# Kernel optimization log

Measured on AMD Instinct MI355X. Metric: run time of the kernel, lower is better.

Reference implementation:

```python
import jax, jax.numpy as jnp
import numpy as np

B, S, H = 1, 4096, 2048
NH, NKV, HD = 8, 4, 256
I = 8192
EPS = 1e-6
THETA = 10000.0
WINDOW = 4096  # hardcoded sliding window for even layer_idx
LAYER_IDX = 0


def rms_norm(x, w):
    v = jnp.mean(jnp.square(x), axis=-1, keepdims=True)
    return x * jax.lax.rsqrt(v + EPS) * w


def rotate_half(x):
    h = x.shape[-1] // 2
    return jnp.concatenate([-x[..., h:], x[..., :h]], axis=-1)


def apply_rope(q, k, positions):
    # q: [B,S,NH,HD], k: [B,S,NKV,HD], positions: [B,S]
    inv_freq = 1.0 / (THETA ** (jnp.arange(0, HD, 2, dtype=jnp.float32) / HD))
    freqs = positions.astype(jnp.float32)[..., None] * inv_freq  # [B,S,HD/2]
    emb = jnp.concatenate([freqs, freqs], axis=-1)               # [B,S,HD]
    cos = jnp.cos(emb)[:, :, None, :]
    sin = jnp.sin(emb)[:, :, None, :]
    q = q * cos + rotate_half(q) * sin
    k = k * cos + rotate_half(k) * sin
    return q, k


def forward(hidden_states, q_w, k_w, v_w, o_w, gate_w, up_w, down_w, ln1_w, ln2_w,
            attention_mask, position_ids):
    # ---- input RMSNorm + attention ----
    residual = hidden_states
    x = rms_norm(hidden_states, ln1_w)

    q = (x @ q_w).reshape(B, S, NH, HD)
    k = (x @ k_w).reshape(B, S, NKV, HD)
    v = (x @ v_w).reshape(B, S, NKV, HD)
    q, k = apply_rope(q, k, position_ids)

    # GQA: repeat kv heads to match query heads
    groups = NH // NKV
    k = jnp.repeat(k, groups, axis=2)  # [B,S,NH,HD]
    v = jnp.repeat(v, groups, axis=2)

    # masks: padding mask AND causal AND (even layer) local window of WINDOW
    row = jnp.arange(S)[:, None]
    col = jnp.arange(S)[None, :]
    causal = col <= row                                   # [S,S]
    combined = causal[None, None] & (attention_mask[:, None, None, :] > 0)
    if LAYER_IDX % 2 == 0:
        keep = ~(col <= row - WINDOW)                     # mask out keys older than WINDOW
        combined = combined & keep[None, None]
    neg = jnp.finfo(jnp.float32).min
    bias = jnp.where(combined, 0.0, neg).astype(jnp.float32)  # [B,1,S,S]

    scale = HD ** -0.5
    scores = jnp.einsum('bqhd,bkhd->bhqk', q, k) * scale + bias
    probs = jax.nn.softmax(scores, axis=-1)
    attn = jnp.einsum('bhqk,bkhd->bqhd', probs, v).reshape(B, S, NH * HD)
    attn_out = attn @ o_w

    hidden_states = residual + attn_out

    # ---- post-attention RMSNorm + gated-GeLU MLP ----
    residual = hidden_states
    x = rms_norm(hidden_states, ln2_w)
    mlp = (jax.nn.gelu(x @ gate_w, approximate=True) * (x @ up_w)) @ down_w
    return residual + mlp


def setup_inputs() -> dict:
    key = jax.random.key(0)
    ks = jax.random.split(key, 9)
    std = 0.02
    n = lambda k, shp: jax.random.normal(k, shp, dtype=jnp.float32) * std
    return {
        'hidden_states': jax.random.normal(ks[0], (B, S, H), dtype=jnp.float32),
        'q_w': n(ks[1], (H, NH * HD)),
        'k_w': n(ks[2], (H, NKV * HD)),
        'v_w': n(ks[3], (H, NKV * HD)),
        'o_w': n(ks[4], (NH * HD, H)),
        'gate_w': n(ks[5], (H, I)),
        'up_w': n(ks[6], (H, I)),
        'down_w': n(ks[7], (I, H)),
        'ln1_w': jnp.ones((H,), jnp.float32),
        'ln2_w': jnp.ones((H,), jnp.float32),
        'attention_mask': jnp.ones((B, S), jnp.int32),
        'position_ids': jnp.broadcast_to(jnp.arange(S, dtype=jnp.int32)[None, :], (B, S)),
    }


def reference(hidden_states, q_w, k_w, v_w, o_w, gate_w, up_w, down_w, ln1_w, ln2_w,
              attention_mask, position_ids):
    return forward(hidden_states, q_w, k_w, v_w, o_w, gate_w, up_w, down_w,
                   ln1_w, ln2_w, attention_mask, position_ids)
```

## Files before the change

### kernel.cpp

```cpp
#include <hip/hip_runtime.h>
#include <hip/hip_bf16.h>
#include <math.h>

#define S_LEN 4096
#define HID   2048
#define NHEADS 8
#define NKVH   4
#define HDIM   256
#define FFN    8192
#define WIN    4096

typedef __bf16 bf16_t;
typedef __bf16 bf16x4 __attribute__((ext_vector_type(4)));
typedef __bf16 bf16x8 __attribute__((ext_vector_type(8)));
typedef float  floatx4 __attribute__((ext_vector_type(4)));

__device__ inline float waveReduceSum(float v) {
#pragma unroll
    for (int o = 32; o > 0; o >>= 1) v += __shfl_xor(v, o);
    return v;
}
__device__ inline float blockReduceSum(float v, float* sh) {
    int tid = threadIdx.x;
    v = waveReduceSum(v);
    if ((tid & 63) == 0) sh[tid >> 6] = v;
    __syncthreads();
    v = sh[0] + sh[1] + sh[2] + sh[3];
    __syncthreads();
    return v;
}

template <typename T>
__global__ __launch_bounds__(256) void transpose_bf16_kernel(const T* __restrict__ in,
                                                             bf16_t* __restrict__ out,
                                                             int R, int C) {
    __shared__ float tile[32][33];
    int tx = threadIdx.x & 31;
    int ty = threadIdx.x >> 5;
    int c0 = blockIdx.x * 32;
    int r0 = blockIdx.y * 32;
#pragma unroll
    for (int i = 0; i < 4; ++i)
        tile[ty + i * 8][tx] = (float)in[(long long)(r0 + ty + i * 8) * C + c0 + tx];
    __syncthreads();
#pragma unroll
    for (int i = 0; i < 4; ++i)
        out[(long long)(c0 + ty + i * 8) * R + r0 + tx] = (bf16_t)tile[tx][ty + i * 8];
}

__global__ __launch_bounds__(256) void rmsnorm_kernel(const float* __restrict__ x,
                                                      const float* __restrict__ w,
                                                      bf16_t* __restrict__ out) {
    __shared__ float sh[4];
    int row = blockIdx.x;
    const float* xr = x + (long long)row * HID;
    float v[8];
    float ss = 0.f;
#pragma unroll
    for (int i = 0; i < 8; ++i) {
        v[i] = xr[threadIdx.x + i * 256];
        ss += v[i] * v[i];
    }
    ss = blockReduceSum(ss, sh);
    float sc = rsqrtf(ss * (1.0f / HID) + 1e-6f);
#pragma unroll
    for (int i = 0; i < 8; ++i) {
        int c = threadIdx.x + i * 256;
        out[(long long)row * HID + c] = (bf16_t)(v[i] * sc * w[c]);
    }
}

__global__ __launch_bounds__(256) void rope_kernel(bf16_t* __restrict__ q,
                                                   bf16_t* __restrict__ k,
                                                   const int* __restrict__ pos_ids) {
    int s = blockIdx.x;
    float p = (float)pos_ids[s];
    for (int t = threadIdx.x; t < (NHEADS + NKVH) * (HDIM / 2); t += 256) {
        int head = t >> 7;
        int i = t & 127;
        float inv = expf(-(2.0f * (float)i / (float)HDIM) * 9.210340371976184f);
        float f = p * inv;
        float sn, cs;
        sincosf(f, &sn, &cs);
        bf16_t* base = (head < NHEADS) ? (q + (long long)s * HID + head * HDIM)
                                       : (k + (long long)s * (NKVH * HDIM) + (head - NHEADS) * HDIM);
        float a = (float)base[i];
        float b = (float)base[i + 128];
        base[i]       = (bf16_t)(a * cs - b * sn);
        base[i + 128] = (bf16_t)(b * cs + a * sn);
    }
}

__global__ __launch_bounds__(256) void flash_attn_kernel(const bf16_t* __restrict__ qg,
                                                         const bf16_t* __restrict__ kg,
                                                         const bf16_t* __restrict__ vTg,
                                                         bf16_t* __restrict__ op0,
                                                         bf16_t* __restrict__ op1,
                                                         float* __restrict__ mlb,
                                                         const int* __restrict__ amask) {
    __shared__ bf16_t sK[64 * 256];
    __shared__ bf16_t sV[256 * 64];

    const int h = blockIdx.y;
    const int kh = blockIdx.z;
    const int tid = threadIdx.x;
    const int lane = tid & 63;
    const int w = tid >> 6;
    const int tl = lane & 15;
    const int quad = lane >> 4;

    const bf16_t* Qh = qg + h * HDIM;
    const bf16_t* Kh = kg + (h >> 1) * HDIM;
    const bf16_t* Vh = vTg + (long long)(h >> 1) * HDIM * S_LEN;
    bf16_t* Op = kh ? op1 : op0;
    bf16_t* sP = sK + w * (16 * 72);

#pragma unroll 1
    for (int half = 0; half < 2; ++half) {
        const int qi = half ? (63 - blockIdx.x) : blockIdx.x;
        const int qr0 = qi * 64;
        const int ntiles = qi + 1;
        const int mid = ntiles >> 1;
        const int t0 = kh ? mid : 0;
        const int t1 = kh ? ntiles : mid;
        const int irow = qr0 + w * 16 + tl;

        const bf16_t* qrow = Qh + (long long)irow * HID;
        bf16x8 qf[8];
#pragma unroll
        for (int ks = 0; ks < 8; ++ks)
            qf[ks] = *(const bf16x8*)(qrow + (ks * 4 + quad) * 8);

        floatx4 oacc[16] = {};
        float m_i = -3e38f, l_i = 0.f;

        for (int t = t0; t < t1; ++t) {
            const int kt = t * 64;
#pragma unroll
            for (int it = 0; it < 8; ++it) {
                int s = it * 256 + tid;
                {
                    int m = s >> 5, sg = s & 31, g = sg ^ (m & 7);
                    const bf16_t* src = Kh + (long long)(kt + m) * (NKVH * HDIM) + g * 8;
                    __builtin_amdgcn_global_load_lds((const __attribute__((address_space(1))) void*)src,
                                                     (__attribute__((address_space(3))) void*)(sK + s * 8),
                                                     16, 0, 0);
                }
                {
                    int m = s >> 3, sg = s & 7, g = sg ^ (m & 7);
                    const bf16_t* src = Vh + (long long)m * S_LEN + kt + g * 8;
                    __builtin_amdgcn_global_load_lds((const __attribute__((address_space(1))) void*)src,
                                                     (__attribute__((address_space(3))) void*)(sV + s * 8),
                                                     16, 0, 0);
                }
            }
            __builtin_amdgcn_s_waitcnt(0x0f70);
            __syncthreads();

            floatx4 sacc[4] = {};
#pragma unroll
            for (int ks = 0; ks < 8; ++ks) {
                bf16x8 kf[4];
#pragma unroll
                for (int ni = 0; ni < 4; ++ni) {
                    int row = ni * 16 + tl;
                    int ph = (ks * 4 + quad) ^ (row & 7);
                    kf[ni] = *(const bf16x8*)(sK + row * 256 + ph * 8);
                }
#pragma unroll
                for (int ni = 0; ni < 4; ++ni)
                    sacc[ni] = __builtin_amdgcn_mfma_f32_16x16x32_bf16(kf[ni], qf[ks], sacc[ni], 0, 0, 0);
            }
            __syncthreads();

            float sv[4][4];
            float mx = -3e38f;
#pragma unroll
            for (int ni = 0; ni < 4; ++ni) {
                int4 am = *(const int4*)(amask + kt + ni * 16 + quad * 4);
#pragma unroll
                for (int r = 0; r < 4; ++r) {
                    int j = kt + ni * 16 + quad * 4 + r;
                    int amr = (r == 0) ? am.x : (r == 1) ? am.y : (r == 2) ? am.z : am.w;
                    bool valid = (j <= irow) && (j > irow - WIN) && (amr > 0);
                    float x = valid ? sacc[ni][r] * 0.0625f : -3e38f;
                    sv[ni][r] = x;
                    mx = fmaxf(mx, x);
                }
            }
            mx = fmaxf(mx, __shfl_xor(mx, 16));
            mx = fmaxf(mx, __shfl_xor(mx, 32));
            float mnew = fmaxf(m_i, mx);
            float alpha = __expf(m_i - mnew);
            float rs = 0.f;
#pragma unroll
            for (int ni = 0; ni < 4; ++ni) {
                bf16x4 pk;
#pragma unroll
                for (int r = 0; r < 4; ++r) {
                    float p = (sv[ni][r] > -1e37f) ? __expf(sv[ni][r] - mnew) : 0.f;
                    rs += p;
                    pk[r] = (bf16_t)p;
                }
                *(bf16x4*)(sP + tl * 72 + ni * 16 + quad * 4) = pk;
            }
            rs += __shfl_xor(rs, 16);
            rs += __shfl_xor(rs, 32);
            l_i = l_i * alpha + rs;
            m_i = mnew;

            floatx4 av;
#pragma unroll
            for (int r = 0; r < 4; ++r) av[r] = __shfl(alpha, quad * 4 + r);
#pragma unroll
            for (int dt = 0; dt < 16; ++dt) oacc[dt] *= av;

#pragma unroll
            for (int k2 = 0; k2 < 2; ++k2) {
                bf16x8 pf = *(const bf16x8*)(sP + tl * 72 + k2 * 32 + quad * 8);
#pragma unroll
                for (int dt = 0; dt < 16; ++dt) {
                    int d = dt * 16 + tl;
                    int ph = (k2 * 4 + quad) ^ (d & 7);
                    bf16x8 vf = *(const bf16x8*)(sV + d * 64 + ph * 8);
                    oacc[dt] = __builtin_amdgcn_mfma_f32_16x16x32_bf16(pf, vf, oacc[dt], 0, 0, 0);
                }
            }
            __syncthreads();
        }

        floatx4 inv;
#pragma unroll
        for (int r = 0; r < 4; ++r) {
            float lv = __shfl(l_i, quad * 4 + r);
            inv[r] = (lv > 0.f) ? 1.0f / lv : 0.f;
        }
#pragma unroll
        for (int dt = 0; dt < 16; ++dt) {
#pragma unroll
            for (int r = 0; r < 4; ++r) {
                long long row = qr0 + w * 16 + quad * 4 + r;
                Op[row * HID + h * HDIM + dt * 16 + tl] = (bf16_t)(oacc[dt][r] * inv[r]);
            }
        }
        if (quad == 0) {
            long long mi = ((long long)(kh * NHEADS + h) * S_LEN + qr0 + w * 16 + tl) * 2;
            mlb[mi] = m_i;
            mlb[mi + 1] = l_i;
        }
    }
}

__global__ __launch_bounds__(256) void combine_kernel(bf16_t* __restrict__ op0,
                                                      const bf16_t* __restrict__ op1,
                                                      const float* __restrict__ mlb) {
    int h = blockIdx.x;
    int row = blockIdx.y;
    int d = threadIdx.x;
    long long m0i = ((long long)h * S_LEN + row) * 2;
    long long m1i = ((long long)(NHEADS + h) * S_LEN + row) * 2;
    float m0 = mlb[m0i], l0 = mlb[m0i + 1];
    float m1 = mlb[m1i], l1 = mlb[m1i + 1];
    float M = fmaxf(m0, m1);
    float w0 = (l0 > 0.f) ? l0 * __expf(m0 - M) : 0.f;
    float w1 = (l1 > 0.f) ? l1 * __expf(m1 - M) : 0.f;
    float inv = 1.0f / (w0 + w1);
    long long idx = (long long)row * HID + h * HDIM + d;
    float v = (w0 * (float)op0[idx] + w1 * (float)op1[idx]) * inv;
    op0[idx] = (bf16_t)v;
}

template <int MODE>
__global__ __launch_bounds__(256) void gemm_kernel(const bf16_t* __restrict__ A, int lda,
                                                   const bf16_t* __restrict__ Bt, int ldb,
                                                   void* __restrict__ Cv, int ldc,
                                                   const void* __restrict__ aux, int K) {
    __shared__ bf16_t smem[2 * 128 * 64];
    bf16_t* sA = smem;
    bf16_t* sB = smem + 128 * 64;

    const int tid = threadIdx.x;
    const int n0 = blockIdx.x * 128;
    const int m0 = blockIdx.y * 128;

    const int lane = tid & 63;
    const int wid = tid >> 6;
    const int wm = (wid >> 1) * 64;
    const int wn = (wid & 1) * 64;
    const int tl = lane & 15;
    const int quad = lane >> 4;

    floatx4 acc[4][4] = {};

    for (int k0 = 0; k0 < K; k0 += 64) {
#pragma unroll
        for (int it = 0; it < 4; ++it) {
            int s = it * 256 + tid;
            int m = s >> 3;
            int sg = s & 7;
            int g = sg ^ (m & 7);
            const bf16_t* ga = A + (long long)(m0 + m) * lda + k0 + g * 8;
            __builtin_amdgcn_global_load_lds((const __attribute__((address_space(1))) void*)ga,
                                             (__attribute__((address_space(3))) void*)(sA + s * 8),
                                             16, 0, 0);
            const bf16_t* gb = Bt + (long long)(n0 + m) * ldb + k0 + g * 8;
            __builtin_amdgcn_global_load_lds((const __attribute__((address_space(1))) void*)gb,
                                             (__attribute__((address_space(3))) void*)(sB + s * 8),
                                             16, 0, 0);
        }
        __builtin_amdgcn_s_waitcnt(0x0f70);
        __syncthreads();

#pragma unroll
        for (int kk = 0; kk < 2; ++kk) {
            bf16x8 af[4], bfr[4];
#pragma unroll
            for (int mi = 0; mi < 4; ++mi) {
                int m = wm + mi * 16 + tl;
                int sg = (kk * 4 + quad) ^ (m & 7);
                af[mi] = *(const bf16x8*)(sA + m * 64 + sg * 8);
            }
#pragma unroll
            for (int ni = 0; ni < 4; ++ni) {
                int n = wn + ni * 16 + tl;
                int sg = (kk * 4 + quad) ^ (n & 7);
                bfr[ni] = *(const bf16x8*)(sB + n * 64 + sg * 8);
            }
#pragma unroll
            for (int mi = 0; mi < 4; ++mi)
#pragma unroll
                for (int ni = 0; ni < 4; ++ni)
                    acc[mi][ni] = __builtin_amdgcn_mfma_f32_16x16x32_bf16(af[mi], bfr[ni], acc[mi][ni], 0, 0, 0);
        }
        __syncthreads();
    }

#pragma unroll
    for (int mi = 0; mi < 4; ++mi) {
#pragma unroll
        for (int ni = 0; ni < 4; ++ni) {
#pragma unroll
            for (int r = 0; r < 4; ++r) {
                int gr = m0 + wm + mi * 16 + quad * 4 + r;
                int gc = n0 + wn + ni * 16 + tl;
                long long idx = (long long)gr * ldc + gc;
                float v = acc[mi][ni][r];
                if (MODE == 0) {
                    ((bf16_t*)Cv)[idx] = (bf16_t)v;
                } else if (MODE == 1) {
                    ((float*)Cv)[idx] = ((const float*)aux)[idx] + v;
                } else {
                    float g = (float)((const bf16_t*)aux)[idx];
                    float t = 0.7978845608028654f * (g + 0.044715f * g * g * g);
                    float ge = 0.5f * g * (1.0f + tanhf(t));
                    ((bf16_t*)Cv)[idx] = (bf16_t)(ge * v);
                }
            }
        }
    }
}

extern "C" void kernel_launch(void* const* d_in, const int* in_sizes, int n_in,
                              void* d_out, int out_size, void* d_ws, size_t ws_size,
                              hipStream_t stream) {
    const float* hidden = (const float*)d_in[0];
    const float* q_w    = (const float*)d_in[1];
    const float* k_w    = (const float*)d_in[2];
    const float* v_w    = (const float*)d_in[3];
    const float* o_w    = (const float*)d_in[4];
    const float* gate_w = (const float*)d_in[5];
    const float* up_w   = (const float*)d_in[6];
    const float* down_w = (const float*)d_in[7];
    const float* ln1_w  = (const float*)d_in[8];
    const float* ln2_w  = (const float*)d_in[9];
    const int* amask    = (const int*)d_in[10];
    const int* pos_ids  = (const int*)d_in[11];
    float* out = (float*)d_out;

    const size_t MB = 1ull << 20;
    char* ws = (char*)d_ws;
    bf16_t* wqT = (bf16_t*)(ws + 0 * MB);
    bf16_t* wkT = (bf16_t*)(ws + 8 * MB);
    bf16_t* wvT = (bf16_t*)(ws + 12 * MB);
    bf16_t* woT = (bf16_t*)(ws + 16 * MB);
    bf16_t* wgT = (bf16_t*)(ws + 24 * MB);
    bf16_t* wuT = (bf16_t*)(ws + 56 * MB);
    bf16_t* wdT = (bf16_t*)(ws + 88 * MB);
    bf16_t* xb    = (bf16_t*)(ws + 120 * MB);
    bf16_t* qb    = (bf16_t*)(ws + 136 * MB);
    bf16_t* kb    = (bf16_t*)(ws + 152 * MB);
    bf16_t* vb    = (bf16_t*)(ws + 160 * MB);
    bf16_t* vT    = (bf16_t*)(ws + 168 * MB);
    bf16_t* op0   = (bf16_t*)(ws + 120 * MB);
    bf16_t* op1   = (bf16_t*)(ws + 176 * MB);
    float*  mlb   = (float*) (ws + 192 * MB);
    bf16_t* attnb = (bf16_t*)(ws + 120 * MB);
    bf16_t* xb2   = (bf16_t*)(ws + 120 * MB);
    bf16_t* gateb = (bf16_t*)(ws + 136 * MB);
    (void)ws_size; (void)in_sizes; (void)n_in; (void)out_size;

    dim3 blk(256);

    transpose_bf16_kernel<float><<<dim3(64, 64), blk, 0, stream>>>(q_w, wqT, 2048, 2048);
    transpose_bf16_kernel<float><<<dim3(32, 64), blk, 0, stream>>>(k_w, wkT, 2048, 1024);
    transpose_bf16_kernel<float><<<dim3(32, 64), blk, 0, stream>>>(v_w, wvT, 2048, 1024);
    transpose_bf16_kernel<float><<<dim3(64, 64), blk, 0, stream>>>(o_w, woT, 2048, 2048);
    transpose_bf16_kernel<float><<<dim3(256, 64), blk, 0, stream>>>(gate_w, wgT, 2048, 8192);
    transpose_bf16_kernel<float><<<dim3(256, 64), blk, 0, stream>>>(up_w, wuT, 2048, 8192);
    transpose_bf16_kernel<float><<<dim3(64, 256), blk, 0, stream>>>(down_w, wdT, 8192, 2048);

    rmsnorm_kernel<<<dim3(S_LEN), blk, 0, stream>>>(hidden, ln1_w, xb);

    gemm_kernel<0><<<dim3(16, 32), blk, 0, stream>>>(xb, HID, wqT, HID, qb, 2048, nullptr, HID);
    gemm_kernel<0><<<dim3(8, 32), blk, 0, stream>>>(xb, HID, wkT, HID, kb, 1024, nullptr, HID);
    gemm_kernel<0><<<dim3(8, 32), blk, 0, stream>>>(xb, HID, wvT, HID, vb, 1024, nullptr, HID);

    rope_kernel<<<dim3(S_LEN), blk, 0, stream>>>(qb, kb, pos_ids);

    transpose_bf16_kernel<bf16_t><<<dim3(32, 128), blk, 0, stream>>>(vb, vT, S_LEN, 1024);

    flash_attn_kernel<<<dim3(32, NHEADS, 2), blk, 0, stream>>>(qb, kb, vT, op0, op1, mlb, amask);
    combine_kernel<<<dim3(NHEADS, S_LEN), blk, 0, stream>>>(op0, op1, mlb);

    gemm_kernel<1><<<dim3(16, 32), blk, 0, stream>>>(attnb, 2048, woT, 2048, out, 2048, hidden, 2048);

    rmsnorm_kernel<<<dim3(S_LEN), blk, 0, stream>>>(out, ln2_w, xb2);

    gemm_kernel<0><<<dim3(64, 32), blk, 0, stream>>>(xb2, HID, wgT, HID, gateb, FFN, nullptr, HID);
    gemm_kernel<2><<<dim3(64, 32), blk, 0, stream>>>(xb2, HID, wuT, HID, gateb, FFN, gateb, HID);
    gemm_kernel<1><<<dim3(16, 32), blk, 0, stream>>>(gateb, FFN, wdT, FFN, out, 2048, out, FFN);
}
```

Before: 1.304 ms.

## Restructure flash attention to 128-row tiles with 4-way KV split, MFMA-fragment LDS layout, chunked MLP

Flash attention now processes 128 query rows per block, with each wave handling two 16-row subtiles that share K/V fragments. The KV range is split four ways instead of two, and combine merges four partial results. The rescale step is skipped when no row maximum increases. K/V and GEMM tiles are now loaded into LDS in MFMA-fragment order, replacing the XOR swizzle so each fragment read is one contiguous per-lane load. The MLP is split into two 4096-column chunks to reuse a smaller intermediate buffer, and the workspace is reordered so the MLP weight transposes run after attention.

```diff
diff --git a/kernel.cpp b/kernel.cpp
--- a/kernel.cpp
+++ b/kernel.cpp
@@ -91,18 +91,17 @@
     }
 }
 
-__global__ __launch_bounds__(256) void flash_attn_kernel(const bf16_t* __restrict__ qg,
-                                                         const bf16_t* __restrict__ kg,
-                                                         const bf16_t* __restrict__ vTg,
-                                                         bf16_t* __restrict__ op0,
-                                                         bf16_t* __restrict__ op1,
-                                                         float* __restrict__ mlb,
-                                                         const int* __restrict__ amask) {
+__global__ __launch_bounds__(256, 2) void flash_attn_kernel(const bf16_t* __restrict__ qg,
+                                                            const bf16_t* __restrict__ kg,
+                                                            const bf16_t* __restrict__ vTg,
+                                                            bf16_t* __restrict__ opb,
+                                                            float* __restrict__ mlb,
+                                                            const int* __restrict__ amask) {
     __shared__ bf16_t sK[64 * 256];
     __shared__ bf16_t sV[256 * 64];
 
     const int h = blockIdx.y;
-    const int kh = blockIdx.z;
+    const int jq = blockIdx.z;
     const int tid = threadIdx.x;
     const int lane = tid & 63;
     const int w = tid >> 6;
@@ -112,162 +111,186 @@
     const bf16_t* Qh = qg + h * HDIM;
     const bf16_t* Kh = kg + (h >> 1) * HDIM;
     const bf16_t* Vh = vTg + (long long)(h >> 1) * HDIM * S_LEN;
-    bf16_t* Op = kh ? op1 : op0;
-    bf16_t* sP = sK + w * (16 * 72);
+    bf16_t* Op = opb + (long long)jq * (S_LEN * HID);
+    float* mlj = mlb + (long long)jq * (NHEADS * S_LEN * 2);
+    bf16_t* sP = sK + w * (32 * 72);
 
 #pragma unroll 1
     for (int half = 0; half < 2; ++half) {
-        const int qi = half ? (63 - blockIdx.x) : blockIdx.x;
-        const int qr0 = qi * 64;
-        const int ntiles = qi + 1;
-        const int mid = ntiles >> 1;
-        const int t0 = kh ? mid : 0;
-        const int t1 = kh ? ntiles : mid;
-        const int irow = qr0 + w * 16 + tl;
-
-        const bf16_t* qrow = Qh + (long long)irow * HID;
-        bf16x8 qf[8];
-#pragma unroll
-        for (int ks = 0; ks < 8; ++ks)
-            qf[ks] = *(const bf16x8*)(qrow + (ks * 4 + quad) * 8);
-
-        floatx4 oacc[16] = {};
-        float m_i = -3e38f, l_i = 0.f;
+        const int qi = half ? (31 - blockIdx.x) : blockIdx.x;
+        const int qr0 = qi * 128;
+        const int T = 2 * qi + 2;
+        const int t0 = (T * jq) >> 2;
+        const int t1 = (T * (jq + 1)) >> 2;
+        const int irow = qr0 + w * 32 + tl;
+
+        bf16x8 qf[2][8];
+#pragma unroll
+        for (int s = 0; s < 2; ++s) {
+            const bf16_t* qrow = Qh + (long long)(irow + s * 16) * HID;
+#pragma unroll
+            for (int ks = 0; ks < 8; ++ks)
+                qf[s][ks] = *(const bf16x8*)(qrow + (ks * 4 + quad) * 8);
+        }
+
+        floatx4 oacc[2][16] = {};
+        float m_i[2] = {-3e38f, -3e38f};
+        float l_i[2] = {0.f, 0.f};
 
         for (int t = t0; t < t1; ++t) {
             const int kt = t * 64;
 #pragma unroll
             for (int it = 0; it < 8; ++it) {
-                int s = it * 256 + tid;
+                int f = it * 4 + w;
                 {
-                    int m = s >> 5, sg = s & 31, g = sg ^ (m & 7);
-                    const bf16_t* src = Kh + (long long)(kt + m) * (NKVH * HDIM) + g * 8;
+                    int row = (f & 3) * 16 + tl;
+                    int dc = (f >> 2) * 4 + quad;
+                    const bf16_t* src = Kh + (long long)(kt + row) * (NKVH * HDIM) + dc * 8;
                     __builtin_amdgcn_global_load_lds((const __attribute__((address_space(1))) void*)src,
-                                                     (__attribute__((address_space(3))) void*)(sK + s * 8),
+                                                     (__attribute__((address_space(3))) void*)(sK + (it * 256 + tid) * 8),
                                                      16, 0, 0);
                 }
                 {
-                    int m = s >> 3, sg = s & 7, g = sg ^ (m & 7);
-                    const bf16_t* src = Vh + (long long)m * S_LEN + kt + g * 8;
+                    int d = (f & 15) * 16 + tl;
+                    int kc = (f >> 4) * 4 + quad;
+                    const bf16_t* src = Vh + (long long)d * S_LEN + kt + kc * 8;
                     __builtin_amdgcn_global_load_lds((const __attribute__((address_space(1))) void*)src,
-                                                     (__attribute__((address_space(3))) void*)(sV + s * 8),
+                                                     (__attribute__((address_space(3))) void*)(sV + (it * 256 + tid) * 8),
                                                      16, 0, 0);
                 }
             }
             __builtin_amdgcn_s_waitcnt(0x0f70);
             __syncthreads();
 
-            floatx4 sacc[4] = {};
+            floatx4 sacc[2][4] = {};
 #pragma unroll
             for (int ks = 0; ks < 8; ++ks) {
-                bf16x8 kf[4];
 #pragma unroll
                 for (int ni = 0; ni < 4; ++ni) {
-                    int row = ni * 16 + tl;
-                    int ph = (ks * 4 + quad) ^ (row & 7);
-                    kf[ni] = *(const bf16x8*)(sK + row * 256 + ph * 8);
-                }
-#pragma unroll
-                for (int ni = 0; ni < 4; ++ni)
-                    sacc[ni] = __builtin_amdgcn_mfma_f32_16x16x32_bf16(kf[ni], qf[ks], sacc[ni], 0, 0, 0);
+                    bf16x8 kf = *(const bf16x8*)(sK + ((ks * 4 + ni) * 64 + lane) * 8);
+                    sacc[0][ni] = __builtin_amdgcn_mfma_f32_16x16x32_bf16(kf, qf[0][ks], sacc[0][ni], 0, 0, 0);
+                    sacc[1][ni] = __builtin_amdgcn_mfma_f32_16x16x32_bf16(kf, qf[1][ks], sacc[1][ni], 0, 0, 0);
+                }
             }
             __syncthreads();
 
-            float sv[4][4];
-            float mx = -3e38f;
-#pragma unroll
-            for (int ni = 0; ni < 4; ++ni) {
-                int4 am = *(const int4*)(amask + kt + ni * 16 + quad * 4);
+            int4 am4[4];
+#pragma unroll
+            for (int ni = 0; ni < 4; ++ni) am4[ni] = *(const int4*)(amask + kt + ni * 16 + quad * 4);
+#pragma unroll
+            for (int s = 0; s < 2; ++s) {
+                const int ir = irow + s * 16;
+                float sv[4][4];
+                float mx = -3e38f;
+#pragma unroll
+                for (int ni = 0; ni < 4; ++ni) {
+#pragma unroll
+                    for (int r = 0; r < 4; ++r) {
+                        int jk = kt + ni * 16 + quad * 4 + r;
+                        int amr = (r == 0) ? am4[ni].x : (r == 1) ? am4[ni].y : (r == 2) ? am4[ni].z : am4[ni].w;
+                        bool valid = (jk <= ir) && (jk > ir - WIN) && (amr > 0);
+                        float x = valid ? sacc[s][ni][r] * 0.0625f : -3e38f;
+                        sv[ni][r] = x;
+                        mx = fmaxf(mx, x);
+                    }
+                }
+                mx = fmaxf(mx, __shfl_xor(mx, 16));
+                mx = fmaxf(mx, __shfl_xor(mx, 32));
+                if (__any(mx > m_i[s])) {
+                    float mnew = fmaxf(m_i[s], mx);
+                    float alpha = __expf(m_i[s] - mnew);
+                    m_i[s] = mnew;
+                    l_i[s] *= alpha;
+                    floatx4 av;
+#pragma unroll
+                    for (int r = 0; r < 4; ++r) av[r] = __shfl(alpha, quad * 4 + r);
+#pragma unroll
+                    for (int dt = 0; dt < 16; ++dt) oacc[s][dt] *= av;
+                }
+                float rs = 0.f;
+#pragma unroll
+                for (int ni = 0; ni < 4; ++ni) {
+                    bf16x4 pk;
+#pragma unroll
+                    for (int r = 0; r < 4; ++r) {
+                        float p = (sv[ni][r] > -1e37f) ? __expf(sv[ni][r] - m_i[s]) : 0.f;
+                        rs += p;
+                        pk[r] = (bf16_t)p;
+                    }
+                    *(bf16x4*)(sP + (s * 16 + tl) * 72 + ni * 16 + quad * 4) = pk;
+                }
+                rs += __shfl_xor(rs, 16);
+                rs += __shfl_xor(rs, 32);
+                l_i[s] += rs;
+            }
+
+#pragma unroll
+            for (int k2 = 0; k2 < 2; ++k2) {
+                bf16x8 pf0 = *(const bf16x8*)(sP + tl * 72 + k2 * 32 + quad * 8);
+                bf16x8 pf1 = *(const bf16x8*)(sP + (16 + tl) * 72 + k2 * 32 + quad * 8);
+#pragma unroll
+                for (int dt = 0; dt < 16; ++dt) {
+                    bf16x8 vf = *(const bf16x8*)(sV + ((k2 * 16 + dt) * 64 + lane) * 8);
+                    oacc[0][dt] = __builtin_amdgcn_mfma_f32_16x16x32_bf16(pf0, vf, oacc[0][dt], 0, 0, 0);
+                    oacc[1][dt] = __builtin_amdgcn_mfma_f32_16x16x32_bf16(pf1, vf, oacc[1][dt], 0, 0, 0);
+                }
+            }
+            __syncthreads();
+        }
+
+#pragma unroll
+        for (int s = 0; s < 2; ++s) {
+            floatx4 inv;
+#pragma unroll
+            for (int r = 0; r < 4; ++r) {
+                float lv = __shfl(l_i[s], quad * 4 + r);
+                inv[r] = (lv > 0.f) ? 1.0f / lv : 0.f;
+            }
+#pragma unroll
+            for (int dt = 0; dt < 16; ++dt) {
 #pragma unroll
                 for (int r = 0; r < 4; ++r) {
-                    int j = kt + ni * 16 + quad * 4 + r;
-                    int amr = (r == 0) ? am.x : (r == 1) ? am.y : (r == 2) ? am.z : am.w;
-                    bool valid = (j <= irow) && (j > irow - WIN) && (amr > 0);
-                    float x = valid ? sacc[ni][r] * 0.0625f : -3e38f;
-                    sv[ni][r] = x;
-                    mx = fmaxf(mx, x);
-                }
-            }
-            mx = fmaxf(mx, __shfl_xor(mx, 16));
-            mx = fmaxf(mx, __shfl_xor(mx, 32));
-            float mnew = fmaxf(m_i, mx);
-            float alpha = __expf(m_i - mnew);
-            float rs = 0.f;
-#pragma unroll
-            for (int ni = 0; ni < 4; ++ni) {
-                bf16x4 pk;
-#pragma unroll
-                for (int r = 0; r < 4; ++r) {
-                    float p = (sv[ni][r] > -1e37f) ? __expf(sv[ni][r] - mnew) : 0.f;
-                    rs += p;
-                    pk[r] = (bf16_t)p;
-                }
-                *(bf16x4*)(sP + tl * 72 + ni * 16 + quad * 4) = pk;
-            }
-            rs += __shfl_xor(rs, 16);
-            rs += __shfl_xor(rs, 32);
-            l_i = l_i * alpha + rs;
-            m_i = mnew;
-
-            floatx4 av;
-#pragma unroll
-            for (int r = 0; r < 4; ++r) av[r] = __shfl(alpha, quad * 4 + r);
-#pragma unroll
-            for (int dt = 0; dt < 16; ++dt) oacc[dt] *= av;
-
-#pragma unroll
-            for (int k2 = 0; k2 < 2; ++k2) {
-                bf16x8 pf = *(const bf16x8*)(sP + tl * 72 + k2 * 32 + quad * 8);
-#pragma unroll
-                for (int dt = 0; dt < 16; ++dt) {
-                    int d = dt * 16 + tl;
-                    int ph = (k2 * 4 + quad) ^ (d & 7);
-                    bf16x8 vf = *(const bf16x8*)(sV + d * 64 + ph * 8);
-                    oacc[dt] = __builtin_amdgcn_mfma_f32_16x16x32_bf16(pf, vf, oacc[dt], 0, 0, 0);
-                }
-            }
-            __syncthreads();
-        }
-
-        floatx4 inv;
-#pragma unroll
-        for (int r = 0; r < 4; ++r) {
-            float lv = __shfl(l_i, quad * 4 + r);
-            inv[r] = (lv > 0.f) ? 1.0f / lv : 0.f;
-        }
-#pragma unroll
-        for (int dt = 0; dt < 16; ++dt) {
-#pragma unroll
-            for (int r = 0; r < 4; ++r) {
-                long long row = qr0 + w * 16 + quad * 4 + r;
-                Op[row * HID + h * HDIM + dt * 16 + tl] = (bf16_t)(oacc[dt][r] * inv[r]);
-            }
-        }
-        if (quad == 0) {
-            long long mi = ((long long)(kh * NHEADS + h) * S_LEN + qr0 + w * 16 + tl) * 2;
-            mlb[mi] = m_i;
-            mlb[mi + 1] = l_i;
-        }
-    }
-}
-
-__global__ __launch_bounds__(256) void combine_kernel(bf16_t* __restrict__ op0,
-                                                      const bf16_t* __restrict__ op1,
-                                                      const float* __restrict__ mlb) {
+                    long long row = qr0 + w * 32 + s * 16 + quad * 4 + r;
+                    Op[row * HID + h * HDIM + dt * 16 + tl] = (bf16_t)(oacc[s][dt][r] * inv[r]);
+                }
+            }
+            if (quad == 0) {
+                long long mi2 = ((long long)h * S_LEN + irow + s * 16) * 2;
+                mlj[mi2] = m_i[s];
+                mlj[mi2 + 1] = l_i[s];
+            }
+        }
+    }
+}
+
+__global__ __launch_bounds__(256) void combine_kernel(const bf16_t* __restrict__ opb,
+                                                      const float* __restrict__ mlb,
+                                                      bf16_t* __restrict__ attnb) {
     int h = blockIdx.x;
     int row = blockIdx.y;
     int d = threadIdx.x;
-    long long m0i = ((long long)h * S_LEN + row) * 2;
-    long long m1i = ((long long)(NHEADS + h) * S_LEN + row) * 2;
-    float m0 = mlb[m0i], l0 = mlb[m0i + 1];
-    float m1 = mlb[m1i], l1 = mlb[m1i + 1];
-    float M = fmaxf(m0, m1);
-    float w0 = (l0 > 0.f) ? l0 * __expf(m0 - M) : 0.f;
-    float w1 = (l1 > 0.f) ? l1 * __expf(m1 - M) : 0.f;
-    float inv = 1.0f / (w0 + w1);
+    float m[4], l[4];
+    float M = -3e38f;
+#pragma unroll
+    for (int j = 0; j < 4; ++j) {
+        long long mi = (((long long)j * NHEADS + h) * S_LEN + row) * 2;
+        m[j] = mlb[mi];
+        l[j] = mlb[mi + 1];
+        M = fmaxf(M, m[j]);
+    }
+    float wj[4], wsum = 0.f;
+#pragma unroll
+    for (int j = 0; j < 4; ++j) {
+        wj[j] = (l[j] > 0.f) ? l[j] * __expf(m[j] - M) : 0.f;
+        wsum += wj[j];
+    }
+    float inv = 1.0f / wsum;
     long long idx = (long long)row * HID + h * HDIM + d;
-    float v = (w0 * (float)op0[idx] + w1 * (float)op1[idx]) * inv;
-    op0[idx] = (bf16_t)v;
+    float acc = 0.f;
+#pragma unroll
+    for (int j = 0; j < 4; ++j)
+        acc += wj[j] * (float)opb[(long long)j * (S_LEN * HID) + idx];
+    attnb[idx] = (bf16_t)(acc * inv);
 }
 
 template <int MODE>
@@ -295,17 +318,16 @@
     for (int k0 = 0; k0 < K; k0 += 64) {
 #pragma unroll
         for (int it = 0; it < 4; ++it) {
-            int s = it * 256 + tid;
-            int m = s >> 3;
-            int sg = s & 7;
-            int g = sg ^ (m & 7);
-            const bf16_t* ga = A + (long long)(m0 + m) * lda + k0 + g * 8;
+            int f = it * 4 + wid;
+            int row = (f & 7) * 16 + tl;
+            int kc = (f >> 3) * 4 + quad;
+            const bf16_t* ga = A + (long long)(m0 + row) * lda + k0 + kc * 8;
             __builtin_amdgcn_global_load_lds((const __attribute__((address_space(1))) void*)ga,
-                                             (__attribute__((address_space(3))) void*)(sA + s * 8),
+                                             (__attribute__((address_space(3))) void*)(sA + (it * 256 + tid) * 8),
                                              16, 0, 0);
-            const bf16_t* gb = Bt + (long long)(n0 + m) * ldb + k0 + g * 8;
+            const bf16_t* gb = Bt + (long long)(n0 + row) * ldb + k0 + kc * 8;
             __builtin_amdgcn_global_load_lds((const __attribute__((address_space(1))) void*)gb,
-                                             (__attribute__((address_space(3))) void*)(sB + s * 8),
+                                             (__attribute__((address_space(3))) void*)(sB + (it * 256 + tid) * 8),
                                              16, 0, 0);
         }
         __builtin_amdgcn_s_waitcnt(0x0f70);
@@ -315,17 +337,11 @@
         for (int kk = 0; kk < 2; ++kk) {
             bf16x8 af[4], bfr[4];
 #pragma unroll
-            for (int mi = 0; mi < 4; ++mi) {
-                int m = wm + mi * 16 + tl;
-                int sg = (kk * 4 + quad) ^ (m & 7);
-                af[mi] = *(const bf16x8*)(sA + m * 64 + sg * 8);
-            }
-#pragma unroll
-            for (int ni = 0; ni < 4; ++ni) {
-                int n = wn + ni * 16 + tl;
-                int sg = (kk * 4 + quad) ^ (n & 7);
-                bfr[ni] = *(const bf16x8*)(sB + n * 64 + sg * 8);
-            }
+            for (int mi = 0; mi < 4; ++mi)
+                af[mi] = *(const bf16x8*)(sA + ((kk * 8 + (wm >> 4) + mi) * 64 + lane) * 8);
+#pragma unroll
+            for (int ni = 0; ni < 4; ++ni)
+                bfr[ni] = *(const bf16x8*)(sB + ((kk * 8 + (wn >> 4) + ni) * 64 + lane) * 8);
 #pragma unroll
             for (int mi = 0; mi < 4; ++mi)
 #pragma unroll
@@ -379,24 +395,23 @@
 
     const size_t MB = 1ull << 20;
     char* ws = (char*)d_ws;
-    bf16_t* wqT = (bf16_t*)(ws + 0 * MB);
-    bf16_t* wkT = (bf16_t*)(ws + 8 * MB);
-    bf16_t* wvT = (bf16_t*)(ws + 12 * MB);
-    bf16_t* woT = (bf16_t*)(ws + 16 * MB);
-    bf16_t* wgT = (bf16_t*)(ws + 24 * MB);
-    bf16_t* wuT = (bf16_t*)(ws + 56 * MB);
-    bf16_t* wdT = (bf16_t*)(ws + 88 * MB);
-    bf16_t* xb    = (bf16_t*)(ws + 120 * MB);
-    bf16_t* qb    = (bf16_t*)(ws + 136 * MB);
-    bf16_t* kb    = (bf16_t*)(ws + 152 * MB);
-    bf16_t* vb    = (bf16_t*)(ws + 160 * MB);
-    bf16_t* vT    = (bf16_t*)(ws + 168 * MB);
-    bf16_t* op0   = (bf16_t*)(ws + 120 * MB);
-    bf16_t* op1   = (bf16_t*)(ws + 176 * MB);
-    float*  mlb   = (float*) (ws + 192 * MB);
-    bf16_t* attnb = (bf16_t*)(ws + 120 * MB);
-    bf16_t* xb2   = (bf16_t*)(ws + 120 * MB);
-    bf16_t* gateb = (bf16_t*)(ws + 136 * MB);
+    bf16_t* wqT   = (bf16_t*)(ws + 0 * MB);
+    bf16_t* wkT   = (bf16_t*)(ws + 8 * MB);
+    bf16_t* wvT   = (bf16_t*)(ws + 12 * MB);
+    bf16_t* woT   = (bf16_t*)(ws + 16 * MB);
+    bf16_t* xb    = (bf16_t*)(ws + 24 * MB);
+    bf16_t* qb    = (bf16_t*)(ws + 40 * MB);
+    bf16_t* kb    = (bf16_t*)(ws + 56 * MB);
+    bf16_t* vb    = (bf16_t*)(ws + 64 * MB);
+    bf16_t* vT    = (bf16_t*)(ws + 72 * MB);
+    bf16_t* opb   = (bf16_t*)(ws + 80 * MB);
+    float*  mlb   = (float*) (ws + 144 * MB);
+    bf16_t* attnb = (bf16_t*)(ws + 24 * MB);
+    bf16_t* xb2   = (bf16_t*)(ws + 48 * MB);
+    bf16_t* wgT   = (bf16_t*)(ws + 64 * MB);
+    bf16_t* wuT   = (bf16_t*)(ws + 96 * MB);
+    bf16_t* wdT   = (bf16_t*)(ws + 128 * MB);
+    bf16_t* gb    = (bf16_t*)(ws + 160 * MB);
     (void)ws_size; (void)in_sizes; (void)n_in; (void)out_size;
 
     dim3 blk(256);
@@ -405,28 +420,34 @@
     transpose_bf16_kernel<float><<<dim3(32, 64), blk, 0, stream>>>(k_w, wkT, 2048, 1024);
     transpose_bf16_kernel<float><<<dim3(32, 64), blk, 0, stream>>>(v_w, wvT, 2048, 1024);
     transpose_bf16_kernel<float><<<dim3(64, 64), blk, 0, stream>>>(o_w, woT, 2048, 2048);
+
+    rmsnorm_kernel<<<dim3(S_LEN), blk, 0, stream>>>(hidden, ln1_w, xb);
+
+    gemm_kernel<0><<<dim3(16, 32), blk, 0, stream>>>(xb, HID, wqT, HID, qb, 2048, nullptr, HID);
+    gemm_kernel<0><<<dim3(8, 32), blk, 0, stream>>>(xb, HID, wkT, HID, kb, 1024, nullptr, HID);
+    gemm_kernel<0><<<dim3(8, 32), blk, 0, stream>>>(xb, HID, wvT, HID, vb, 1024, nullptr, HID);
+
+    rope_kernel<<<dim3(S_LEN), blk, 0, stream>>>(qb, kb, pos_ids);
+
+    transpose_bf16_kernel<bf16_t><<<dim3(32, 128), blk, 0, stream>>>(vb, vT, S_LEN, 1024);
+
+    flash_attn_kernel<<<dim3(16, NHEADS, 4), blk, 0, stream>>>(qb, kb, vT, opb, mlb, amask);
+    combine_kernel<<<dim3(NHEADS, S_LEN), blk, 0, stream>>>(opb, mlb, attnb);
+
+    gemm_kernel<1><<<dim3(16, 32), blk, 0, stream>>>(attnb, 2048, woT, 2048, out, 2048, hidden, 2048);
+
+    rmsnorm_kernel<<<dim3(S_LEN), blk, 0, stream>>>(out, ln2_w, xb2);
+
     transpose_bf16_kernel<float><<<dim3(256, 64), blk, 0, stream>>>(gate_w, wgT, 2048, 8192);
     transpose_bf16_kernel<float><<<dim3(256, 64), blk, 0, stream>>>(up_w, wuT, 2048, 8192);
     transpose_bf16_kernel<float><<<dim3(64, 256), blk, 0, stream>>>(down_w, wdT, 8192, 2048);
 
-    rmsnorm_kernel<<<dim3(S_LEN), blk, 0, stream>>>(hidden, ln1_w, xb);
-
-    gemm_kernel<0><<<dim3(16, 32), blk, 0, stream>>>(xb, HID, wqT, HID, qb, 2048, nullptr, HID);
-    gemm_kernel<0><<<dim3(8, 32), blk, 0, stream>>>(xb, HID, wkT, HID, kb, 1024, nullptr, HID);
-    gemm_kernel<0><<<dim3(8, 32), blk, 0, stream>>>(xb, HID, wvT, HID, vb, 1024, nullptr, HID);
-
-    rope_kernel<<<dim3(S_LEN), blk, 0, stream>>>(qb, kb, pos_ids);
-
-    transpose_bf16_kernel<bf16_t><<<dim3(32, 128), blk, 0, stream>>>(vb, vT, S_LEN, 1024);
-
-    flash_attn_kernel<<<dim3(32, NHEADS, 2), blk, 0, stream>>>(qb, kb, vT, op0, op1, mlb, amask);
-    combine_kernel<<<dim3(NHEADS, S_LEN), blk, 0, stream>>>(op0, op1, mlb);
-
-    gemm_kernel<1><<<dim3(16, 32), blk, 0, stream>>>(attnb, 2048, woT, 2048, out, 2048, hidden, 2048);
-
-    rmsnorm_kernel<<<dim3(S_LEN), blk, 0, stream>>>(out, ln2_w, xb2);
-
-    gemm_kernel<0><<<dim3(64, 32), blk, 0, stream>>>(xb2, HID, wgT, HID, gateb, FFN, nullptr, HID);
-    gemm_kernel<2><<<dim3(64, 32), blk, 0, stream>>>(xb2, HID, wuT, HID, gateb, FFN, gateb, HID);
-    gemm_kernel<1><<<dim3(16, 32), blk, 0, stream>>>(gateb, FFN, wdT, FFN, out, 2048, out, FFN);
-}
+    for (int c = 0; c < 2; ++c) {
+        bf16_t* wgc = wgT + (size_t)c * 4096 * HID;
+        bf16_t* wuc = wuT + (size_t)c * 4096 * HID;
+        bf16_t* wdc = wdT + (size_t)c * 4096;
+        gemm_kernel<0><<<dim3(32, 32), blk, 0, stream>>>(xb2, HID, wgc, HID, gb, 4096, nullptr, HID);
+        gemm_kernel<2><<<dim3(32, 32), blk, 0, stream>>>(xb2, HID, wuc, HID, gb, 4096, gb, HID);
+        gemm_kernel<1><<<dim3(16, 32), blk, 0, stream>>>(gb, 4096, wdc, FFN, out, 2048, out, 4096);
+    }
+}
```

Measured after the change: 1.673 ms. +28.2%, slower.
